# Kernel optimization log

Hardware: AMD Instinct MI355X
Metric: run time of the kernel (lower is better)

Reference implementation:

```python
import jax, jax.numpy as jnp
import numpy as np


def _mlp2(x, w1, b1, w2, b2):
    # two-linear MLP with tanh after each layer (Sequential(MLP, activation))
    h = jnp.tanh(x @ w1.T + b1)
    return jnp.tanh(h @ w2.T + b2)


def setup_inputs() -> dict:
    key = jax.random.key(0)
    ks = jax.random.split(key, 12)
    N, K, D, H, C = 20000, 32, 128, 128, 64
    s = 0.1
    return {
        "z": jax.random.normal(ks[0], (N, D), jnp.float32),
        "z_": jax.random.normal(ks[1], (N, K, D), jnp.float32),
        "cur_w1": s * jax.random.normal(ks[2], (H, D), jnp.float32),
        "cur_b1": jax.random.uniform(ks[3], (H,), jnp.float32, -0.1, 0.1),
        "cur_w2": s * jax.random.normal(ks[4], (H, H), jnp.float32),
        "cur_b2": jax.random.uniform(ks[5], (H,), jnp.float32, -0.1, 0.1),
        "nbr_w1": s * jax.random.normal(ks[6], (H, 2 * D), jnp.float32),
        "nbr_b1": jax.random.uniform(ks[7], (H,), jnp.float32, -0.1, 0.1),
        "nbr_w2": s * jax.random.normal(ks[8], (H, H), jnp.float32),
        "nbr_b2": jax.random.uniform(ks[9], (H,), jnp.float32, -0.1, 0.1),
        "out_w": s * jax.random.normal(ks[10], (C, 2 * H), jnp.float32),
        "out_b": jax.random.uniform(ks[11], (C,), jnp.float32, -0.1, 0.1),
    }


def reference(z, z_, cur_w1, cur_b1, cur_w2, cur_b2,
              nbr_w1, nbr_b1, nbr_w2, nbr_b2, out_w, out_b):
    N, K, D = z_.shape
    # current-node branch: [N, H]
    v = _mlp2(z, cur_w1, cur_b1, cur_w2, cur_b2)
    # neighbor branch: repeat z over K, concat with z_ -> [N, K, 2D]
    zc = jnp.concatenate([jnp.broadcast_to(z[:, None, :], (N, K, D)), z_], axis=2)
    vn = _mlp2(zc, nbr_w1, nbr_b1, nbr_w2, nbr_b2)  # [N, K, H]
    v_ = vn.sum(axis=1)  # sum-aggregate over neighbors -> [N, H]
    # output linear on concatenated features -> [N, dim_c]
    dc = jnp.concatenate([v, v_], axis=1) @ out_w.T + out_b
    return dc
```

## Files before the change

### kernel.cpp

```cpp
#include <hip/hip_runtime.h>


typedef __bf16 bf16;
typedef __bf16 bf16x2 __attribute__((ext_vector_type(2)));
typedef __bf16 bf16x8 __attribute__((ext_vector_type(8)));
typedef float  f32x4  __attribute__((ext_vector_type(4)));

#define MFMA(a, b, c) __builtin_amdgcn_mfma_f32_16x16x32_bf16((a), (b), (c), 0, 0, 0)

__device__ __forceinline__ void block_sync_lds() {
    asm volatile("s_waitcnt lgkmcnt(0)\n\ts_barrier" ::: "memory");
}

__device__ __forceinline__ float fast_tanh(float x) {
    float ax = __builtin_fabsf(x);
    float t  = __builtin_amdgcn_exp2f(ax * 2.885390081777927f);
    float r  = 1.0f - 2.0f * __builtin_amdgcn_rcpf(t + 1.0f);
    return __builtin_copysignf(r, x);
}

__device__ __forceinline__ bf16x8 cvt8(f32x4 a, f32x4 b) {
    bf16x8 r;
    r[0] = (bf16)a[0]; r[1] = (bf16)a[1]; r[2] = (bf16)a[2]; r[3] = (bf16)a[3];
    r[4] = (bf16)b[0]; r[5] = (bf16)b[1]; r[6] = (bf16)b[2]; r[7] = (bf16)b[3];
    return r;
}

__device__ __forceinline__ int swz128(int row, int col) {
    int c = (col >> 3) ^ (row & 15);
    return row * 256 + c * 16 + (col & 7) * 2;
}
__device__ __forceinline__ int swz256(int row, int col) {
    int c = (col >> 3) ^ (row & 15);
    return row * 512 + c * 16 + (col & 7) * 2;
}

__device__ __forceinline__ void st_pair(char* base, int off, float a, float b) {
    bf16x2 p = {(bf16)a, (bf16)b};
    *(bf16x2*)(base + off) = p;
}

__global__ __launch_bounds__(256, 2) void nbr_kernel(
    const float* __restrict__ zn, const float* __restrict__ u1,
    const float* __restrict__ w1, const float* __restrict__ w2,
    const float* __restrict__ b2,
    bf16* __restrict__ feat, int NP)
{
    __shared__ char zc_lds[2][32 * 256];
    __shared__ char h1_lds[2][32 * 256];

    const int t = threadIdx.x;
    const int wv = t >> 6, lane = t & 63, g = lane >> 4, li = lane & 15;
    const int hbase = wv * 32;

    bf16x8 w1f[2][4];
#pragma unroll
    for (int ht = 0; ht < 2; ++ht)
#pragma unroll
        for (int kb = 0; kb < 4; ++kb) {
            const float* p = w1 + (size_t)(hbase + 16*ht + li) * 256 + 128 + kb*32 + 8*g;
            w1f[ht][kb] = cvt8(*(const f32x4*)p, *(const f32x4*)(p + 4));
        }
    bf16x8 w2f[2][4];
#pragma unroll
    for (int nt = 0; nt < 2; ++nt)
#pragma unroll
        for (int kb = 0; kb < 4; ++kb) {
            const float* p = w2 + (size_t)(hbase + 16*nt + li) * 128 + kb*32 + 8*g;
            w2f[nt][kb] = cvt8(*(const f32x4*)p, *(const f32x4*)(p + 4));
        }
    float b2v[2];
#pragma unroll
    for (int nt = 0; nt < 2; ++nt) b2v[nt] = b2[hbase + 16*nt + li];

    const int sm  = t >> 3;
    const int scf = (t & 7) * 16;
    const int stride = gridDim.x;

    f32x4 r[2][4];
    f32x4 uu[2][2];
    {
        int p = blockIdx.x;
#pragma unroll
        for (int j = 0; j < 2; ++j) {
            const float* src = zn + ((size_t)(2*p + j) * 32 + sm) * 128 + scf;
#pragma unroll
            for (int q = 0; q < 4; ++q) r[j][q] = *(const f32x4*)(src + 4*q);
#pragma unroll
            for (int ht = 0; ht < 2; ++ht)
                uu[j][ht] = *(const f32x4*)(u1 + (size_t)(2*p + j) * 128 + hbase + 16*ht + 4*g);
        }
    }

    const f32x4 vzero = {0.f, 0.f, 0.f, 0.f};

    for (int p = blockIdx.x; p < NP; p += stride) {
#pragma unroll
        for (int j = 0; j < 2; ++j) {
            *(bf16x8*)(zc_lds[j] + swz128(sm, scf))     = cvt8(r[j][0], r[j][1]);
            *(bf16x8*)(zc_lds[j] + swz128(sm, scf + 8)) = cvt8(r[j][2], r[j][3]);
        }
        block_sync_lds();

        const int pp = p + stride;
        if (pp < NP) {
#pragma unroll
            for (int j = 0; j < 2; ++j) {
                const float* src = zn + ((size_t)(2*pp + j) * 32 + sm) * 128 + scf;
#pragma unroll
                for (int q = 0; q < 4; ++q) r[j][q] = *(const f32x4*)(src + 4*q);
            }
        }

        f32x4 acc1[2][2][2];
#pragma unroll
        for (int j = 0; j < 2; ++j)
#pragma unroll
            for (int a = 0; a < 2; ++a)
#pragma unroll
                for (int b = 0; b < 2; ++b) acc1[j][a][b] = vzero;

        __builtin_amdgcn_s_setprio(1);
#pragma unroll
        for (int kb = 0; kb < 4; ++kb) {
            bf16x8 bz[2][2];
#pragma unroll
            for (int j = 0; j < 2; ++j)
#pragma unroll
                for (int mt = 0; mt < 2; ++mt)
                    bz[j][mt] = *(const bf16x8*)(zc_lds[j] + swz128(16*mt + li, kb*32 + 8*g));
#pragma unroll
            for (int j = 0; j < 2; ++j)
#pragma unroll
                for (int ht = 0; ht < 2; ++ht)
#pragma unroll
                    for (int mt = 0; mt < 2; ++mt)
                        acc1[j][ht][mt] = MFMA(w1f[ht][kb], bz[j][mt], acc1[j][ht][mt]);
        }
        __builtin_amdgcn_s_setprio(0);

#pragma unroll
        for (int j = 0; j < 2; ++j)
#pragma unroll
            for (int ht = 0; ht < 2; ++ht)
#pragma unroll
                for (int mt = 0; mt < 2; ++mt) {
                    float v0 = fast_tanh(acc1[j][ht][mt][0] + uu[j][ht][0]);
                    float v1 = fast_tanh(acc1[j][ht][mt][1] + uu[j][ht][1]);
                    float v2 = fast_tanh(acc1[j][ht][mt][2] + uu[j][ht][2]);
                    float v3 = fast_tanh(acc1[j][ht][mt][3] + uu[j][ht][3]);
                    int m = 16*mt + li;
                    int h = hbase + 16*ht + 4*g;
                    st_pair(h1_lds[j], swz128(m, h),     v0, v1);
                    st_pair(h1_lds[j], swz128(m, h + 2), v2, v3);
                }

        if (pp < NP) {
#pragma unroll
            for (int j = 0; j < 2; ++j)
#pragma unroll
                for (int ht = 0; ht < 2; ++ht)
                    uu[j][ht] = *(const f32x4*)(u1 + (size_t)(2*pp + j) * 128 + hbase + 16*ht + 4*g);
        }
        block_sync_lds();

        f32x4 acc2[2][2][2];
#pragma unroll
        for (int j = 0; j < 2; ++j)
#pragma unroll
            for (int a = 0; a < 2; ++a)
#pragma unroll
                for (int b = 0; b < 2; ++b) acc2[j][a][b] = vzero;

        __builtin_amdgcn_s_setprio(1);
#pragma unroll
        for (int kb = 0; kb < 4; ++kb) {
            bf16x8 ah[2][2];
#pragma unroll
            for (int j = 0; j < 2; ++j)
#pragma unroll
                for (int mt = 0; mt < 2; ++mt)
                    ah[j][mt] = *(const bf16x8*)(h1_lds[j] + swz128(16*mt + li, kb*32 + 8*g));
#pragma unroll
            for (int j = 0; j < 2; ++j)
#pragma unroll
                for (int mt = 0; mt < 2; ++mt)
#pragma unroll
                    for (int nt = 0; nt < 2; ++nt)
                        acc2[j][mt][nt] = MFMA(ah[j][mt], w2f[nt][kb], acc2[j][mt][nt]);
        }
        __builtin_amdgcn_s_setprio(0);

#pragma unroll
        for (int j = 0; j < 2; ++j) {
            float s0 = 0.f, s1 = 0.f;
#pragma unroll
            for (int mt = 0; mt < 2; ++mt)
#pragma unroll
                for (int rr = 0; rr < 4; ++rr) {
                    s0 += fast_tanh(acc2[j][mt][0][rr] + b2v[0]);
                    s1 += fast_tanh(acc2[j][mt][1][rr] + b2v[1]);
                }
            s0 += __shfl_xor(s0, 16); s0 += __shfl_xor(s0, 32);
            s1 += __shfl_xor(s1, 16); s1 += __shfl_xor(s1, 32);
            if (lane < 16) {
                bf16* dst = feat + (size_t)(2*p + j) * 256 + 128 + hbase + lane;
                dst[0]  = (bf16)s0;
                dst[16] = (bf16)s1;
            }
        }
    }
}

__global__ __launch_bounds__(256, 2) void cur_kernel(
    const float* __restrict__ z,
    const float* __restrict__ w1, const float* __restrict__ b1,
    const float* __restrict__ w2, const float* __restrict__ b2,
    const float* __restrict__ nw1, const float* __restrict__ nb1,
    bf16* __restrict__ feat, float* __restrict__ u1, int N)
{
    __shared__ char z_lds[64 * 256];
    __shared__ char h1_lds[64 * 256];

    const int t = threadIdx.x;
    const int wv = t >> 6, lane = t & 63, g = lane >> 4, li = lane & 15;
    const int hbase = wv * 32;
    const int n0 = blockIdx.x * 64;

    bf16x8 w1f[2][4], w2f[2][4], wzf[2][4];
#pragma unroll
    for (int ht = 0; ht < 2; ++ht)
#pragma unroll
        for (int kb = 0; kb < 4; ++kb) {
            const float* p1 = w1 + (size_t)(hbase + 16*ht + li) * 128 + kb*32 + 8*g;
            w1f[ht][kb] = cvt8(*(const f32x4*)p1, *(const f32x4*)(p1 + 4));
            const float* p2 = w2 + (size_t)(hbase + 16*ht + li) * 128 + kb*32 + 8*g;
            w2f[ht][kb] = cvt8(*(const f32x4*)p2, *(const f32x4*)(p2 + 4));
            const float* p3 = nw1 + (size_t)(hbase + 16*ht + li) * 256 + kb*32 + 8*g;
            wzf[ht][kb] = cvt8(*(const f32x4*)p3, *(const f32x4*)(p3 + 4));
        }
    float b1v[2][4], b2v[2][4], bnv[2][4];
#pragma unroll
    for (int ht = 0; ht < 2; ++ht)
#pragma unroll
        for (int rr = 0; rr < 4; ++rr) {
            b1v[ht][rr] = b1[hbase + 16*ht + 4*g + rr];
            b2v[ht][rr] = b2[hbase + 16*ht + 4*g + rr];
            bnv[ht][rr] = nb1[hbase + 16*ht + 4*g + rr];
        }

    {
        int m = t >> 2;
        int c0 = (t & 3) * 32;
        int row = n0 + m; if (row > N - 1) row = N - 1;
        const float* src = z + (size_t)row * 128 + c0;
#pragma unroll
        for (int q = 0; q < 4; ++q) {
            f32x4 a = *(const f32x4*)(src + 8*q);
            f32x4 b = *(const f32x4*)(src + 8*q + 4);
            *(bf16x8*)(z_lds + swz128(m, c0 + 8*q)) = cvt8(a, b);
        }
    }
    __syncthreads();

    const f32x4 vzero = {0.f, 0.f, 0.f, 0.f};
    f32x4 acc1[2][4], accz[2][4];
#pragma unroll
    for (int a = 0; a < 2; ++a)
#pragma unroll
        for (int b = 0; b < 4; ++b) { acc1[a][b] = vzero; accz[a][b] = vzero; }

#pragma unroll
    for (int kb = 0; kb < 4; ++kb) {
        bf16x8 bz[4];
#pragma unroll
        for (int mt = 0; mt < 4; ++mt)
            bz[mt] = *(const bf16x8*)(z_lds + swz128(16*mt + li, kb*32 + 8*g));
#pragma unroll
        for (int ht = 0; ht < 2; ++ht)
#pragma unroll
            for (int mt = 0; mt < 4; ++mt) {
                acc1[ht][mt] = MFMA(w1f[ht][kb], bz[mt], acc1[ht][mt]);
                accz[ht][mt] = MFMA(wzf[ht][kb], bz[mt], accz[ht][mt]);
            }
    }

#pragma unroll
    for (int ht = 0; ht < 2; ++ht)
#pragma unroll
        for (int mt = 0; mt < 4; ++mt) {
            int row = n0 + 16*mt + li;
            if (row < N) {
                f32x4 v;
#pragma unroll
                for (int rr = 0; rr < 4; ++rr) v[rr] = accz[ht][mt][rr] + bnv[ht][rr];
                *(f32x4*)(u1 + (size_t)row * 128 + hbase + 16*ht + 4*g) = v;
            }
        }

#pragma unroll
    for (int ht = 0; ht < 2; ++ht)
#pragma unroll
        for (int mt = 0; mt < 4; ++mt) {
            float v0 = fast_tanh(acc1[ht][mt][0] + b1v[ht][0]);
            float v1 = fast_tanh(acc1[ht][mt][1] + b1v[ht][1]);
            float v2 = fast_tanh(acc1[ht][mt][2] + b1v[ht][2]);
            float v3 = fast_tanh(acc1[ht][mt][3] + b1v[ht][3]);
            int m = 16*mt + li;
            int h = hbase + 16*ht + 4*g;
            st_pair(h1_lds, swz128(m, h),     v0, v1);
            st_pair(h1_lds, swz128(m, h + 2), v2, v3);
        }
    __syncthreads();

    f32x4 acc2[2][4];
#pragma unroll
    for (int a = 0; a < 2; ++a)
#pragma unroll
        for (int b = 0; b < 4; ++b) acc2[a][b] = vzero;

#pragma unroll
    for (int kb = 0; kb < 4; ++kb) {
        bf16x8 bh[4];
#pragma unroll
        for (int mt = 0; mt < 4; ++mt)
            bh[mt] = *(const bf16x8*)(h1_lds + swz128(16*mt + li, kb*32 + 8*g));
#pragma unroll
        for (int ht = 0; ht < 2; ++ht)
#pragma unroll
            for (int mt = 0; mt < 4; ++mt)
                acc2[ht][mt] = MFMA(w2f[ht][kb], bh[mt], acc2[ht][mt]);
    }
#pragma unroll
    for (int ht = 0; ht < 2; ++ht)
#pragma unroll
        for (int mt = 0; mt < 4; ++mt) {
            float v0 = fast_tanh(acc2[ht][mt][0] + b2v[ht][0]);
            float v1 = fast_tanh(acc2[ht][mt][1] + b2v[ht][1]);
            float v2 = fast_tanh(acc2[ht][mt][2] + b2v[ht][2]);
            float v3 = fast_tanh(acc2[ht][mt][3] + b2v[ht][3]);
            int row = n0 + 16*mt + li;
            if (row < N) {
                int h = hbase + 16*ht + 4*g;
                bf16* dst = feat + (size_t)row * 256 + h;
                bf16x2 p01 = {(bf16)v0, (bf16)v1};
                bf16x2 p23 = {(bf16)v2, (bf16)v3};
                *(bf16x2*)(dst)     = p01;
                *(bf16x2*)(dst + 2) = p23;
            }
        }
}

__global__ __launch_bounds__(256, 2) void out_kernel(
    const bf16* __restrict__ feat,
    const float* __restrict__ ow, const float* __restrict__ ob,
    float* __restrict__ out, int N)
{
    __shared__ char f_lds[64 * 512];

    const int t = threadIdx.x, wv = t >> 6, lane = t & 63, g = lane >> 4, li = lane & 15;
    const int cbase = wv * 16;
    const int n0 = blockIdx.x * 64;

    bf16x8 owf[8];
#pragma unroll
    for (int kb = 0; kb < 8; ++kb) {
        const float* p = ow + (size_t)(cbase + li) * 256 + kb*32 + 8*g;
        owf[kb] = cvt8(*(const f32x4*)p, *(const f32x4*)(p + 4));
    }
    float obv = ob[cbase + li];

    {
        int m = t >> 2;
        int c0 = (t & 3) * 64;
        int row = n0 + m; if (row > N - 1) row = N - 1;
        const bf16* src = feat + (size_t)row * 256 + c0;
#pragma unroll
        for (int q = 0; q < 8; ++q)
            *(bf16x8*)(f_lds + swz256(m, c0 + 8*q)) = *(const bf16x8*)(src + 8*q);
    }
    __syncthreads();

    const f32x4 vzero = {0.f, 0.f, 0.f, 0.f};
    f32x4 acc[4];
#pragma unroll
    for (int a = 0; a < 4; ++a) acc[a] = vzero;

#pragma unroll
    for (int kb = 0; kb < 8; ++kb) {
        bf16x8 af[4];
#pragma unroll
        for (int mt = 0; mt < 4; ++mt)
            af[mt] = *(const bf16x8*)(f_lds + swz256(16*mt + li, kb*32 + 8*g));
#pragma unroll
        for (int mt = 0; mt < 4; ++mt)
            acc[mt] = MFMA(af[mt], owf[kb], acc[mt]);
    }
#pragma unroll
    for (int mt = 0; mt < 4; ++mt)
#pragma unroll
        for (int rr = 0; rr < 4; ++rr) {
            int row = n0 + 16*mt + 4*g + rr;
            if (row < N) out[(size_t)row * 64 + cbase + li] = acc[mt][rr] + obv;
        }
}

extern "C" void kernel_launch(void* const* d_in, const int* in_sizes, int n_in,
                              void* d_out, int out_size, void* d_ws, size_t ws_size,
                              hipStream_t stream) {
    const float* z   = (const float*)d_in[0];
    const float* zn  = (const float*)d_in[1];
    const float* cw1 = (const float*)d_in[2];
    const float* cb1 = (const float*)d_in[3];
    const float* cw2 = (const float*)d_in[4];
    const float* cb2 = (const float*)d_in[5];
    const float* nw1 = (const float*)d_in[6];
    const float* nb1 = (const float*)d_in[7];
    const float* nw2 = (const float*)d_in[8];
    const float* nb2 = (const float*)d_in[9];
    const float* ow  = (const float*)d_in[10];
    const float* ob  = (const float*)d_in[11];
    float* out = (float*)d_out;

    const int N  = in_sizes[0] / 128;
    const int NP = N / 2;
    const int nblk = (N + 63) / 64;

    bf16*  feat = (bf16*)d_ws;
    float* u1   = (float*)((char*)d_ws + (size_t)N * 256 * sizeof(bf16));

    (void)n_in; (void)out_size; (void)ws_size;

    cur_kernel<<<nblk, 256, 0, stream>>>(z, cw1, cb1, cw2, cb2, nw1, nb1, feat, u1, N);
    nbr_kernel<<<512, 256, 0, stream>>>(zn, u1, nw1, nw2, nb2, feat, NP);
    out_kernel<<<nblk, 256, 0, stream>>>(feat, ow, ob, out, N);
}
```

Before: 125.9 us.

## Double-buffer neighbor loads two iterations ahead and streamline tanh arithmetic

The neighbor loop now keeps two register buffers and issues the global load for iteration p+2*stride, so each load has a full iteration of latency cover. The loop is unrolled by two through a lambda. The tanh is simplified by dropping the abs/copysign and folding the bias into an FMA on the exp2 input. The second-layer sum accumulates only the reciprocal part, with 32 - 2*sum applied once at the end. The h1 LDS writes also become single 8-byte stores. In exchange the buffering raises register pressure, and the sign-free tanh can overflow exp2 to inf; rcp(inf) gives 0, so the result still comes out as 1.

```diff
diff --git a/kernel.cpp b/kernel.cpp
--- a/kernel.cpp
+++ b/kernel.cpp
@@ -3,20 +3,29 @@
 
 typedef __bf16 bf16;
 typedef __bf16 bf16x2 __attribute__((ext_vector_type(2)));
+typedef __bf16 bf16x4 __attribute__((ext_vector_type(4)));
 typedef __bf16 bf16x8 __attribute__((ext_vector_type(8)));
 typedef float  f32x4  __attribute__((ext_vector_type(4)));
 
 #define MFMA(a, b, c) __builtin_amdgcn_mfma_f32_16x16x32_bf16((a), (b), (c), 0, 0, 0)
 
+#define C2LOG2E 2.885390081777927f
+
 __device__ __forceinline__ void block_sync_lds() {
     asm volatile("s_waitcnt lgkmcnt(0)\n\ts_barrier" ::: "memory");
 }
 
 __device__ __forceinline__ float fast_tanh(float x) {
-    float ax = __builtin_fabsf(x);
-    float t  = __builtin_amdgcn_exp2f(ax * 2.885390081777927f);
-    float r  = 1.0f - 2.0f * __builtin_amdgcn_rcpf(t + 1.0f);
-    return __builtin_copysignf(r, x);
+    float t = __builtin_amdgcn_exp2f(x * C2LOG2E);
+    return 1.0f - 2.0f * __builtin_amdgcn_rcpf(t + 1.0f);
+}
+__device__ __forceinline__ float fast_tanh_fb(float acc, float uc) {
+    float t = __builtin_amdgcn_exp2f(__builtin_fmaf(acc, C2LOG2E, uc));
+    return 1.0f - 2.0f * __builtin_amdgcn_rcpf(t + 1.0f);
+}
+__device__ __forceinline__ float tanh_rpart(float acc, float uc) {
+    float t = __builtin_amdgcn_exp2f(__builtin_fmaf(acc, C2LOG2E, uc));
+    return __builtin_amdgcn_rcpf(t + 1.0f);
 }
 
 __device__ __forceinline__ bf16x8 cvt8(f32x4 a, f32x4 b) {
@@ -69,48 +78,50 @@
             const float* p = w2 + (size_t)(hbase + 16*nt + li) * 128 + kb*32 + 8*g;
             w2f[nt][kb] = cvt8(*(const f32x4*)p, *(const f32x4*)(p + 4));
         }
-    float b2v[2];
-#pragma unroll
-    for (int nt = 0; nt < 2; ++nt) b2v[nt] = b2[hbase + 16*nt + li];
+    float bc2v[2];
+#pragma unroll
+    for (int nt = 0; nt < 2; ++nt) bc2v[nt] = b2[hbase + 16*nt + li] * C2LOG2E;
 
     const int sm  = t >> 3;
     const int scf = (t & 7) * 16;
-    const int stride = gridDim.x;
-
-    f32x4 r[2][4];
+    const int str = gridDim.x;
+
+    f32x4 rA[2][4], rB[2][4];
     f32x4 uu[2][2];
-    {
-        int p = blockIdx.x;
+
+    auto load_zn = [&](f32x4 (&R)[2][4], int pp) {
 #pragma unroll
         for (int j = 0; j < 2; ++j) {
-            const float* src = zn + ((size_t)(2*p + j) * 32 + sm) * 128 + scf;
-#pragma unroll
-            for (int q = 0; q < 4; ++q) r[j][q] = *(const f32x4*)(src + 4*q);
+            const float* src = zn + ((size_t)(2*pp + j) * 32 + sm) * 128 + scf;
+#pragma unroll
+            for (int q = 0; q < 4; ++q) R[j][q] = *(const f32x4*)(src + 4*q);
+        }
+    };
+    auto load_u = [&](int pp) {
+#pragma unroll
+        for (int j = 0; j < 2; ++j)
 #pragma unroll
             for (int ht = 0; ht < 2; ++ht)
-                uu[j][ht] = *(const f32x4*)(u1 + (size_t)(2*p + j) * 128 + hbase + 16*ht + 4*g);
-        }
-    }
+                uu[j][ht] = *(const f32x4*)(u1 + (size_t)(2*pp + j) * 128 + hbase + 16*ht + 4*g);
+    };
+
+    const int p0 = blockIdx.x;
+    load_zn(rA, p0);
+    if (p0 + str < NP) load_zn(rB, p0 + str);
+    load_u(p0);
 
     const f32x4 vzero = {0.f, 0.f, 0.f, 0.f};
 
-    for (int p = blockIdx.x; p < NP; p += stride) {
+    auto iter_body = [&](f32x4 (&R)[2][4], int p) {
 #pragma unroll
         for (int j = 0; j < 2; ++j) {
-            *(bf16x8*)(zc_lds[j] + swz128(sm, scf))     = cvt8(r[j][0], r[j][1]);
-            *(bf16x8*)(zc_lds[j] + swz128(sm, scf + 8)) = cvt8(r[j][2], r[j][3]);
+            *(bf16x8*)(zc_lds[j] + swz128(sm, scf))     = cvt8(R[j][0], R[j][1]);
+            *(bf16x8*)(zc_lds[j] + swz128(sm, scf + 8)) = cvt8(R[j][2], R[j][3]);
         }
         block_sync_lds();
 
-        const int pp = p + stride;
-        if (pp < NP) {
-#pragma unroll
-            for (int j = 0; j < 2; ++j) {
-                const float* src = zn + ((size_t)(2*pp + j) * 32 + sm) * 128 + scf;
-#pragma unroll
-                for (int q = 0; q < 4; ++q) r[j][q] = *(const f32x4*)(src + 4*q);
-            }
-        }
+        const int pz = p + 2*str;
+        if (pz < NP) load_zn(R, pz);
 
         f32x4 acc1[2][2][2];
 #pragma unroll
@@ -142,26 +153,23 @@
 #pragma unroll
         for (int j = 0; j < 2; ++j)
 #pragma unroll
-            for (int ht = 0; ht < 2; ++ht)
+            for (int ht = 0; ht < 2; ++ht) {
+                f32x4 uc = uu[j][ht] * C2LOG2E;
 #pragma unroll
                 for (int mt = 0; mt < 2; ++mt) {
-                    float v0 = fast_tanh(acc1[j][ht][mt][0] + uu[j][ht][0]);
-                    float v1 = fast_tanh(acc1[j][ht][mt][1] + uu[j][ht][1]);
-                    float v2 = fast_tanh(acc1[j][ht][mt][2] + uu[j][ht][2]);
-                    float v3 = fast_tanh(acc1[j][ht][mt][3] + uu[j][ht][3]);
+                    float v0 = fast_tanh_fb(acc1[j][ht][mt][0], uc[0]);
+                    float v1 = fast_tanh_fb(acc1[j][ht][mt][1], uc[1]);
+                    float v2 = fast_tanh_fb(acc1[j][ht][mt][2], uc[2]);
+                    float v3 = fast_tanh_fb(acc1[j][ht][mt][3], uc[3]);
                     int m = 16*mt + li;
                     int h = hbase + 16*ht + 4*g;
-                    st_pair(h1_lds[j], swz128(m, h),     v0, v1);
-                    st_pair(h1_lds[j], swz128(m, h + 2), v2, v3);
+                    bf16x4 q = {(bf16)v0, (bf16)v1, (bf16)v2, (bf16)v3};
+                    *(bf16x4*)(h1_lds[j] + swz128(m, h)) = q;
                 }
-
-        if (pp < NP) {
-#pragma unroll
-            for (int j = 0; j < 2; ++j)
-#pragma unroll
-                for (int ht = 0; ht < 2; ++ht)
-                    uu[j][ht] = *(const f32x4*)(u1 + (size_t)(2*pp + j) * 128 + hbase + 16*ht + 4*g);
-        }
+            }
+
+        const int pu = p + str;
+        if (pu < NP) load_u(pu);
         block_sync_lds();
 
         f32x4 acc2[2][2][2];
@@ -193,22 +201,32 @@
 
 #pragma unroll
         for (int j = 0; j < 2; ++j) {
-            float s0 = 0.f, s1 = 0.f;
+            float sr0 = 0.f, sr1 = 0.f;
 #pragma unroll
             for (int mt = 0; mt < 2; ++mt)
 #pragma unroll
                 for (int rr = 0; rr < 4; ++rr) {
-                    s0 += fast_tanh(acc2[j][mt][0][rr] + b2v[0]);
-                    s1 += fast_tanh(acc2[j][mt][1][rr] + b2v[1]);
+                    sr0 += tanh_rpart(acc2[j][mt][0][rr], bc2v[0]);
+                    sr1 += tanh_rpart(acc2[j][mt][1][rr], bc2v[1]);
                 }
-            s0 += __shfl_xor(s0, 16); s0 += __shfl_xor(s0, 32);
-            s1 += __shfl_xor(s1, 16); s1 += __shfl_xor(s1, 32);
+            sr0 += __shfl_xor(sr0, 16); sr0 += __shfl_xor(sr0, 32);
+            sr1 += __shfl_xor(sr1, 16); sr1 += __shfl_xor(sr1, 32);
             if (lane < 16) {
+                float s0 = __builtin_fmaf(-2.f, sr0, 32.f);
+                float s1 = __builtin_fmaf(-2.f, sr1, 32.f);
                 bf16* dst = feat + (size_t)(2*p + j) * 256 + 128 + hbase + lane;
                 dst[0]  = (bf16)s0;
                 dst[16] = (bf16)s1;
             }
         }
+    };
+
+    for (int p = p0; p < NP; ) {
+        iter_body(rA, p);
+        p += str;
+        if (p >= NP) break;
+        iter_body(rB, p);
+        p += str;
     }
 }
 
```

Measured after the change: 129.2 us. +2.6%, slower.
